# Performance work log

Hardware: AMD Instinct MI355X
Metric: run time of the kernel (lower is better)

Reference implementation:

```python
import jax, jax.numpy as jnp
import numpy as np

BN_EPS = 1e-5


def _conv_bn_elu(x, w, b, bn_scale, bn_bias, bn_mean, bn_var):
    # 1x1 conv == channel-mixing matmul: x [B,C,H,W], w [O,C]
    y = jnp.einsum('bchw,oc->bohw', x, w) + b[None, :, None, None]
    inv = bn_scale * jax.lax.rsqrt(bn_var + BN_EPS)
    y = y * inv[None, :, None, None] + (bn_bias - bn_mean * inv)[None, :, None, None]
    return jax.nn.elu(y)


def setup_inputs() -> dict:
    key = jax.random.key(0)
    ks = jax.random.split(key, 24)
    B, C, H, W = 4, 128, 64, 64
    d = {}
    d['x_q'] = jax.random.normal(ks[0], (B, C, H, W), jnp.float32)
    d['x_k'] = jax.random.normal(ks[1], (B, C, H, W), jnp.float32)
    d['x_v'] = jax.random.normal(ks[2], (B, C, H, W), jnp.float32)
    scale = 1.0 / np.sqrt(C)
    i = 3
    for p in ('q', 'k', 'v'):
        d[f'{p}_w'] = jax.random.normal(ks[i], (C, C), jnp.float32) * scale; i += 1
        d[f'{p}_b'] = jax.random.normal(ks[i], (C,), jnp.float32) * 0.01; i += 1
        d[f'{p}_bn_scale'] = jnp.ones((C,), jnp.float32) + 0.1 * jax.random.normal(ks[i], (C,), jnp.float32); i += 1
        d[f'{p}_bn_bias'] = 0.1 * jax.random.normal(ks[i], (C,), jnp.float32); i += 1
        d[f'{p}_bn_mean'] = 0.1 * jax.random.normal(ks[i], (C,), jnp.float32); i += 1
        d[f'{p}_bn_var'] = jax.random.uniform(ks[i], (C,), jnp.float32, 0.5, 1.5); i += 1
    # torch inits gamma/beta to zero; use small nonzero values so output is informative
    d['gamma'] = jnp.array([0.5], jnp.float32)
    d['beta'] = jnp.array([0.5], jnp.float32)
    return d


def reference(x_q, x_k, x_v,
              q_w, q_b, q_bn_scale, q_bn_bias, q_bn_mean, q_bn_var,
              k_w, k_b, k_bn_scale, k_bn_bias, k_bn_mean, k_bn_var,
              v_w, v_b, v_bn_scale, v_bn_bias, v_bn_mean, v_bn_var,
              gamma, beta):
    B, C, Hv, Wv = x_v.shape
    q = _conv_bn_elu(x_q, q_w, q_b, q_bn_scale, q_bn_bias, q_bn_mean, q_bn_var).reshape(B, C, -1)  # [B,C,HWq]
    k = _conv_bn_elu(x_k, k_w, k_b, k_bn_scale, k_bn_bias, k_bn_mean, k_bn_var).reshape(B, C, -1)  # [B,C,HWk]
    v = _conv_bn_elu(x_v, v_w, v_b, v_bn_scale, v_bn_bias, v_bn_mean, v_bn_var).reshape(B, C, -1)  # [B,C,HWv]
    energy = jnp.einsum('bcq,bck->bqk', q, k)                 # [B,HWq,HWk] (no scaling, as in source)
    attention = jax.nn.softmax(energy, axis=-1)
    out = jnp.einsum('bck,bqk->bcq', v, attention)            # [B,C,HWq]
    out = out.reshape(B, C, Hv, Wv)
    return gamma * out + beta * x_v
```

## Files before the change

### kernel.cpp

```cpp
#include <hip/hip_runtime.h>

#define CC 128
#define SS 4096
#define L2E 1.44269504f

typedef _Float16 f16;
typedef f16 f16x8 __attribute__((ext_vector_type(8)));
typedef float f32x4 __attribute__((ext_vector_type(4)));

struct PArg { const float *x, *w, *b, *sc, *bb, *bm, *bv; f16* out; };

__global__ __launch_bounds__(256) void projk(PArg A0, PArg A1, PArg A2) {
    const int p = blockIdx.y;
    PArg A = (p == 0) ? A0 : ((p == 1) ? A1 : A2);
    const int bx = blockIdx.x;
    const int b  = bx >> 6;
    const int s0 = (bx & 63) * 64;
    const int tid = threadIdx.x;
    const int w = tid >> 6, lane = tid & 63;
    const int n = lane & 15, g = lane >> 4;

    __shared__ f16 Xl[64][136];
    __shared__ f16 Wl[128][136];
    __shared__ float invA[128], ebA[128];
    f16* Yl = &Wl[0][0];

    if (tid < 128) {
        float iv = A.sc[tid] * rsqrtf(A.bv[tid] + 1e-5f);
        invA[tid] = iv;
        ebA[tid] = (A.b[tid] - A.bm[tid]) * iv + A.bb[tid];
    }
#pragma unroll
    for (int i = 0; i < 8; ++i) {
        int vi = tid + i * 256;
        int c = vi >> 4, sq = (vi & 15) * 4;
        float4 v = *(const float4*)(A.x + ((size_t)b * CC + c) * SS + s0 + sq);
        Xl[sq + 0][c] = (f16)v.x; Xl[sq + 1][c] = (f16)v.y;
        Xl[sq + 2][c] = (f16)v.z; Xl[sq + 3][c] = (f16)v.w;
    }
    __syncthreads();
#pragma unroll
    for (int i = 0; i < 8; ++i) {
        int vi = tid + i * 256;
        int o = vi >> 4, cq = (vi & 15) * 8;
        const float* wp = A.w + o * CC + cq;
        float4 a = *(const float4*)wp;
        float4 b4 = *(const float4*)(wp + 4);
        float iv = invA[o];
        union { f16 h[8]; uint4 u; } pk;
        pk.h[0] = (f16)(a.x * iv);  pk.h[1] = (f16)(a.y * iv);
        pk.h[2] = (f16)(a.z * iv);  pk.h[3] = (f16)(a.w * iv);
        pk.h[4] = (f16)(b4.x * iv); pk.h[5] = (f16)(b4.y * iv);
        pk.h[6] = (f16)(b4.z * iv); pk.h[7] = (f16)(b4.w * iv);
        *(uint4*)&Wl[o][cq] = pk.u;
    }
    __syncthreads();

    if (p < 2) {
        f32x4 acc[2][4];
#pragma unroll
        for (int mt = 0; mt < 2; ++mt)
#pragma unroll
            for (int nt = 0; nt < 4; ++nt) acc[mt][nt] = (f32x4){0.f, 0.f, 0.f, 0.f};
#pragma unroll
        for (int ks = 0; ks < 4; ++ks) {
            f16x8 af[2], bf[4];
#pragma unroll
            for (int mt = 0; mt < 2; ++mt) af[mt] = *(const f16x8*)&Wl[w * 32 + mt * 16 + n][ks * 32 + g * 8];
#pragma unroll
            for (int nt = 0; nt < 4; ++nt) bf[nt] = *(const f16x8*)&Xl[nt * 16 + n][ks * 32 + g * 8];
#pragma unroll
            for (int mt = 0; mt < 2; ++mt)
#pragma unroll
                for (int nt = 0; nt < 4; ++nt)
                    acc[mt][nt] = __builtin_amdgcn_mfma_f32_16x16x32_f16(af[mt], bf[nt], acc[mt][nt], 0, 0, 0);
        }
        __syncthreads();
#pragma unroll
        for (int mt = 0; mt < 2; ++mt) {
            float ebr[4];
#pragma unroll
            for (int r = 0; r < 4; ++r) ebr[r] = ebA[w * 32 + mt * 16 + g * 4 + r];
#pragma unroll
            for (int nt = 0; nt < 4; ++nt) {
                union { f16 h[4]; uint2 u; } pk;
#pragma unroll
                for (int r = 0; r < 4; ++r) {
                    float y = acc[mt][nt][r] + ebr[r];
                    y = (y > 0.f) ? y : (expf(y) - 1.f);
                    pk.h[r] = (f16)y;
                }
                *(uint2*)&Yl[(nt * 16 + n) * 136 + w * 32 + mt * 16 + g * 4] = pk.u;
            }
        }
        __syncthreads();
#pragma unroll
        for (int i = 0; i < 4; ++i) {
            int vi = tid + i * 256;
            int s = vi >> 4, cl = (vi & 15) * 8;
            *(uint4*)&A.out[((size_t)b * SS + s0 + s) * CC + cl] = *(const uint4*)&Yl[s * 136 + cl];
        }
    } else {
        f32x4 acc[8];
#pragma unroll
        for (int nt = 0; nt < 8; ++nt) acc[nt] = (f32x4){0.f, 0.f, 0.f, 0.f};
#pragma unroll
        for (int ks = 0; ks < 4; ++ks) {
            f16x8 af = *(const f16x8*)&Xl[w * 16 + n][ks * 32 + g * 8];
#pragma unroll
            for (int nt = 0; nt < 8; ++nt) {
                f16x8 bf = *(const f16x8*)&Wl[nt * 16 + n][ks * 32 + g * 8];
                acc[nt] = __builtin_amdgcn_mfma_f32_16x16x32_f16(af, bf, acc[nt], 0, 0, 0);
            }
        }
        __syncthreads();
#pragma unroll
        for (int nt = 0; nt < 8; ++nt) {
            float ebc = ebA[nt * 16 + n];
            union { f16 h[4]; uint2 u; } pk;
#pragma unroll
            for (int r = 0; r < 4; ++r) {
                float y = acc[nt][r] + ebc;
                y = (y > 0.f) ? y : (expf(y) - 1.f);
                pk.h[r] = (f16)y;
            }
            *(uint2*)&Yl[(nt * 16 + n) * 136 + w * 16 + g * 4] = pk.u;
        }
        __syncthreads();
#pragma unroll
        for (int i = 0; i < 4; ++i) {
            int vi = tid + i * 256;
            int o = vi >> 3, sl = (vi & 7) * 8;
            *(uint4*)&A.out[((size_t)b * CC + o) * SS + s0 + sl] = *(const uint4*)&Yl[o * 136 + sl];
        }
    }
}

__global__ __launch_bounds__(256, 3) void attnk(
    const f16* __restrict__ Qt, const f16* __restrict__ Kt, const f16* __restrict__ Vt,
    f16* __restrict__ Op, float* __restrict__ Ml)
{
    const int tid = threadIdx.x;
    const int bx = blockIdx.x;
    const int qt = bx & 31;
    const int kh = (bx >> 5) & 7;
    const int b  = bx >> 8;
    const int q0 = qt * 128;
    const int kbeg = kh * 512;

    __shared__ __align__(16) char arena[54272];
    f16 (*Kl)[136] = (f16(*)[136])arena;
    f16 (*Vl)[72]  = (f16(*)[72])(arena + 17408);

    const int w = tid >> 6, lane = tid & 63;
    const int n = lane & 15, g = lane >> 4;
    f16 (*Pw)[72] = (f16(*)[72])(arena + 35840 + w * 4608);

    f16x8 qf[2][4];
    {
        const f16* Qb = Qt + ((size_t)b * SS + q0 + w * 32) * CC;
#pragma unroll
        for (int qt2 = 0; qt2 < 2; ++qt2)
#pragma unroll
            for (int ks = 0; ks < 4; ++ks)
                qf[qt2][ks] = *(const f16x8*)&Qb[(qt2 * 16 + n) * CC + ks * 32 + g * 8];
    }

    f32x4 oacc[8][2];
#pragma unroll
    for (int mtc = 0; mtc < 8; ++mtc)
#pragma unroll
        for (int qt2 = 0; qt2 < 2; ++qt2) oacc[mtc][qt2] = (f32x4){0.f, 0.f, 0.f, 0.f};
    float mreg[2] = {-1e30f, -1e30f}, lsum[2] = {0.f, 0.f};

    for (int kt = 0; kt < 8; ++kt) {
        const int k0 = kbeg + kt * 64;
        __syncthreads();
#pragma unroll
        for (int i = 0; i < 4; ++i) {
            int vi = tid + i * 256;
            int rk = vi >> 4, ck = (vi & 15) * 8;
            *(uint4*)&Kl[rk][ck] = *(const uint4*)&Kt[((size_t)b * SS + k0 + rk) * CC + ck];
            int rv = vi >> 3, cv = (vi & 7) * 8;
            *(uint4*)&Vl[rv][cv] = *(const uint4*)&Vt[((size_t)b * CC + rv) * SS + k0 + cv];
        }
        __syncthreads();

        f32x4 sacc[4][2];
#pragma unroll
        for (int kt2 = 0; kt2 < 4; ++kt2)
#pragma unroll
            for (int qt2 = 0; qt2 < 2; ++qt2) sacc[kt2][qt2] = (f32x4){0.f, 0.f, 0.f, 0.f};
#pragma unroll
        for (int ks = 0; ks < 4; ++ks) {
            f16x8 kf[4];
#pragma unroll
            for (int kt2 = 0; kt2 < 4; ++kt2) kf[kt2] = *(const f16x8*)&Kl[kt2 * 16 + n][ks * 32 + g * 8];
#pragma unroll
            for (int kt2 = 0; kt2 < 4; ++kt2)
#pragma unroll
                for (int qt2 = 0; qt2 < 2; ++qt2)
                    sacc[kt2][qt2] = __builtin_amdgcn_mfma_f32_16x16x32_f16(kf[kt2], qf[qt2][ks], sacc[kt2][qt2], 0, 0, 0);
        }

        float al[2];
#pragma unroll
        for (int qt2 = 0; qt2 < 2; ++qt2) {
            float v = sacc[0][qt2][0];
#pragma unroll
            for (int kt2 = 0; kt2 < 4; ++kt2)
#pragma unroll
                for (int r = 0; r < 4; ++r) v = fmaxf(v, sacc[kt2][qt2][r]);
            v = fmaxf(v, __shfl_xor(v, 16));
            v = fmaxf(v, __shfl_xor(v, 32));
            float mn = fmaxf(mreg[qt2], v);
            al[qt2] = exp2f((mreg[qt2] - mn) * L2E);
            mreg[qt2] = mn;
            float rs = 0.f;
#pragma unroll
            for (int kt2 = 0; kt2 < 4; ++kt2) {
                union { f16 h[4]; uint2 u; } pk;
#pragma unroll
                for (int r = 0; r < 4; ++r) {
                    float p = exp2f((sacc[kt2][qt2][r] - mn) * L2E);
                    rs += p;
                    pk.h[r] = (f16)p;
                }
                *(uint2*)&Pw[qt2 * 16 + n][kt2 * 16 + g * 4] = pk.u;
            }
            lsum[qt2] = lsum[qt2] * al[qt2] + rs;
        }
#pragma unroll
        for (int mtc = 0; mtc < 8; ++mtc)
#pragma unroll
            for (int qt2 = 0; qt2 < 2; ++qt2)
#pragma unroll
                for (int r = 0; r < 4; ++r) oacc[mtc][qt2][r] *= al[qt2];

#pragma unroll
        for (int ks = 0; ks < 2; ++ks) {
            f16x8 vf[8], pf[2];
#pragma unroll
            for (int mtc = 0; mtc < 8; ++mtc) vf[mtc] = *(const f16x8*)&Vl[mtc * 16 + n][ks * 32 + g * 8];
#pragma unroll
            for (int qt2 = 0; qt2 < 2; ++qt2) pf[qt2] = *(const f16x8*)&Pw[qt2 * 16 + n][ks * 32 + g * 8];
#pragma unroll
            for (int mtc = 0; mtc < 8; ++mtc)
#pragma unroll
                for (int qt2 = 0; qt2 < 2; ++qt2)
                    oacc[mtc][qt2] = __builtin_amdgcn_mfma_f32_16x16x32_f16(vf[mtc], pf[qt2], oacc[mtc][qt2], 0, 0, 0);
        }
    }

    float lreg[2];
#pragma unroll
    for (int qt2 = 0; qt2 < 2; ++qt2) {
        float s = lsum[qt2];
        s += __shfl_xor(s, 16);
        s += __shfl_xor(s, 32);
        lreg[qt2] = s;
    }

    const int pidx = (b * 32 + qt) * 8 + kh;
    if (g == 0) {
        float* MlW = Ml + (size_t)pidx * 256;
#pragma unroll
        for (int qt2 = 0; qt2 < 2; ++qt2) {
            int q = w * 32 + qt2 * 16 + n;
            MlW[q]       = mreg[qt2];
            MlW[128 + q] = lreg[qt2];
        }
    }

    __syncthreads();
    f16 (*S2)[136] = (f16(*)[136])arena;
#pragma unroll
    for (int mtc = 0; mtc < 8; ++mtc)
#pragma unroll
        for (int qt2 = 0; qt2 < 2; ++qt2)
#pragma unroll
            for (int r = 0; r < 4; ++r)
                S2[mtc * 16 + g * 4 + r][w * 32 + qt2 * 16 + n] = (f16)oacc[mtc][qt2][r];
    __syncthreads();
    f16* OpW = Op + (size_t)pidx * 16384;
#pragma unroll
    for (int i = 0; i < 8; ++i) {
        int vi = tid + i * 256;
        int c = vi >> 4, qq = (vi & 15) * 8;
        *(uint4*)&OpW[c * 128 + qq] = *(const uint4*)&S2[c][qq];
    }
}

__global__ __launch_bounds__(256) void mrgk(
    const f16* __restrict__ Op, const float* __restrict__ Ml,
    const float* __restrict__ xv, const float* __restrict__ gp, const float* __restrict__ bp,
    float* __restrict__ out)
{
    const int bx = blockIdx.x;
    const int cg = bx & 3, bqt = bx >> 2;
    const int b = bqt >> 5, qt = bqt & 31;
    const int tid = threadIdx.x;
    const int q = tid & 127, hf = tid >> 7;

    const float* ml = Ml + (size_t)bqt * 8 * 256;
    float m = -1e30f;
#pragma unroll
    for (int k2 = 0; k2 < 8; ++k2) m = fmaxf(m, ml[k2 * 256 + q]);
    float wt[8], tot = 0.f;
#pragma unroll
    for (int k2 = 0; k2 < 8; ++k2) {
        wt[k2] = exp2f((ml[k2 * 256 + q] - m) * L2E);
        tot += wt[k2] * ml[k2 * 256 + 128 + q];
    }
    float inv = 1.f / tot;
    float gm = gp[0], bb = bp[0];

    const f16* O = Op + (size_t)bqt * 8 * 16384;
#pragma unroll 2
    for (int i = 0; i < 16; ++i) {
        int c = cg * 32 + hf * 16 + i;
        float o = 0.f;
#pragma unroll
        for (int k2 = 0; k2 < 8; ++k2) o += wt[k2] * (float)O[k2 * 16384 + c * 128 + q];
        o *= inv;
        size_t idx = ((size_t)(b * CC + c)) * SS + qt * 128 + q;
        out[idx] = gm * o + bb * xv[idx];
    }
}

extern "C" void kernel_launch(void* const* d_in, const int* in_sizes, int n_in,
                              void* d_out, int out_size, void* d_ws, size_t ws_size,
                              hipStream_t stream) {
    (void)in_sizes; (void)n_in; (void)out_size; (void)ws_size;

    const size_t TEN = (size_t)4 * SS * CC;
    f16* Qt = (f16*)d_ws;
    f16* Kt = Qt + TEN;
    f16* Vt = Kt + TEN;
    f16* Op = Vt + TEN;
    float* Ml = (float*)(Op + (size_t)1024 * 16384);

    PArg aq = { (const float*)d_in[0], (const float*)d_in[3],  (const float*)d_in[4],
                (const float*)d_in[5], (const float*)d_in[6],  (const float*)d_in[7],
                (const float*)d_in[8],  Qt };
    PArg ak = { (const float*)d_in[1], (const float*)d_in[9],  (const float*)d_in[10],
                (const float*)d_in[11], (const float*)d_in[12], (const float*)d_in[13],
                (const float*)d_in[14], Kt };
    PArg av = { (const float*)d_in[2], (const float*)d_in[15], (const float*)d_in[16],
                (const float*)d_in[17], (const float*)d_in[18], (const float*)d_in[19],
                (const float*)d_in[20], Vt };

    hipLaunchKernelGGL(projk, dim3(256, 3), dim3(256), 0, stream, aq, ak, av);
    hipLaunchKernelGGL(attnk, dim3(1024), dim3(256), 0, stream, Qt, Kt, Vt, Op, Ml);
    hipLaunchKernelGGL(mrgk, dim3(512), dim3(256), 0, stream,
                       Op, Ml, (const float*)d_in[2], (const float*)d_in[21],
                       (const float*)d_in[22], (float*)d_out);
}
```

Measured before the change: 215.9 us.

## Drop split-K attention and merge kernel; fuse epilogue and prefetch K/V tiles

Replaces the split-key flash attention (8 key partitions per query tile plus a separate merge kernel) with one block per 64-query tile that walks all 4096 keys. The gamma/beta epilogue is fused into the attention kernel, so the f16 partial-output workspace and the merge launch go away. K/V tiles for the next step are now prefetched into registers. In exchange the grid shrinks from 1024 to 256 blocks, each wave handles only 16 queries, and per-block serial work is longer, so the GPU may be underoccupied and each K/V tile feeds fewer MFMAs.

```diff
diff --git a/kernel.cpp b/kernel.cpp
--- a/kernel.cpp
+++ b/kernel.cpp
@@ -136,61 +136,74 @@
     }
 }
 
-__global__ __launch_bounds__(256, 3) void attnk(
+__global__ __launch_bounds__(256) void attnk(
     const f16* __restrict__ Qt, const f16* __restrict__ Kt, const f16* __restrict__ Vt,
-    f16* __restrict__ Op, float* __restrict__ Ml)
+    const float* __restrict__ xv, const float* __restrict__ gp, const float* __restrict__ bp,
+    float* __restrict__ out)
 {
     const int tid = threadIdx.x;
     const int bx = blockIdx.x;
-    const int qt = bx & 31;
-    const int kh = (bx >> 5) & 7;
-    const int b  = bx >> 8;
-    const int q0 = qt * 128;
-    const int kbeg = kh * 512;
-
-    __shared__ __align__(16) char arena[54272];
+    const int b  = bx >> 6;
+    const int qt = bx & 63;
+    const int q0 = qt * 64;
+
+    __shared__ __align__(16) char arena[45056];
     f16 (*Kl)[136] = (f16(*)[136])arena;
     f16 (*Vl)[72]  = (f16(*)[72])(arena + 17408);
 
     const int w = tid >> 6, lane = tid & 63;
     const int n = lane & 15, g = lane >> 4;
-    f16 (*Pw)[72] = (f16(*)[72])(arena + 35840 + w * 4608);
-
-    f16x8 qf[2][4];
+    f16 (*Pw)[72] = (f16(*)[72])(arena + 35840 + w * 2304);
+
+    f16x8 qf[4];
     {
-        const f16* Qb = Qt + ((size_t)b * SS + q0 + w * 32) * CC;
-#pragma unroll
-        for (int qt2 = 0; qt2 < 2; ++qt2)
-#pragma unroll
-            for (int ks = 0; ks < 4; ++ks)
-                qf[qt2][ks] = *(const f16x8*)&Qb[(qt2 * 16 + n) * CC + ks * 32 + g * 8];
-    }
-
-    f32x4 oacc[8][2];
-#pragma unroll
-    for (int mtc = 0; mtc < 8; ++mtc)
-#pragma unroll
-        for (int qt2 = 0; qt2 < 2; ++qt2) oacc[mtc][qt2] = (f32x4){0.f, 0.f, 0.f, 0.f};
-    float mreg[2] = {-1e30f, -1e30f}, lsum[2] = {0.f, 0.f};
-
-    for (int kt = 0; kt < 8; ++kt) {
-        const int k0 = kbeg + kt * 64;
+        const f16* Qb = Qt + ((size_t)b * SS + q0 + w * 16 + n) * CC;
+#pragma unroll
+        for (int ks = 0; ks < 4; ++ks)
+            qf[ks] = *(const f16x8*)&Qb[ks * 32 + g * 8];
+    }
+
+    f32x4 oacc[8];
+#pragma unroll
+    for (int mtc = 0; mtc < 8; ++mtc) oacc[mtc] = (f32x4){0.f, 0.f, 0.f, 0.f};
+    float mreg = -1e30f, lsum = 0.f;
+
+    uint4 pk4[4], pv4[4];
+#pragma unroll
+    for (int i = 0; i < 4; ++i) {
+        int vi = tid + i * 256;
+        int rk = vi >> 4, ck = (vi & 15) * 8;
+        pk4[i] = *(const uint4*)&Kt[((size_t)b * SS + rk) * CC + ck];
+        int rv = vi >> 3, cv = (vi & 7) * 8;
+        pv4[i] = *(const uint4*)&Vt[((size_t)b * CC + rv) * SS + cv];
+    }
+
+    for (int kt = 0; kt < 64; ++kt) {
         __syncthreads();
 #pragma unroll
         for (int i = 0; i < 4; ++i) {
             int vi = tid + i * 256;
             int rk = vi >> 4, ck = (vi & 15) * 8;
-            *(uint4*)&Kl[rk][ck] = *(const uint4*)&Kt[((size_t)b * SS + k0 + rk) * CC + ck];
+            *(uint4*)&Kl[rk][ck] = pk4[i];
             int rv = vi >> 3, cv = (vi & 7) * 8;
-            *(uint4*)&Vl[rv][cv] = *(const uint4*)&Vt[((size_t)b * CC + rv) * SS + k0 + cv];
-        }
-        __syncthreads();
-
-        f32x4 sacc[4][2];
-#pragma unroll
-        for (int kt2 = 0; kt2 < 4; ++kt2)
-#pragma unroll
-            for (int qt2 = 0; qt2 < 2; ++qt2) sacc[kt2][qt2] = (f32x4){0.f, 0.f, 0.f, 0.f};
+            *(uint4*)&Vl[rv][cv] = pv4[i];
+        }
+        if (kt < 63) {
+            const int k1 = (kt + 1) * 64;
+#pragma unroll
+            for (int i = 0; i < 4; ++i) {
+                int vi = tid + i * 256;
+                int rk = vi >> 4, ck = (vi & 15) * 8;
+                pk4[i] = *(const uint4*)&Kt[((size_t)b * SS + k1 + rk) * CC + ck];
+                int rv = vi >> 3, cv = (vi & 7) * 8;
+                pv4[i] = *(const uint4*)&Vt[((size_t)b * CC + rv) * SS + k1 + cv];
+            }
+        }
+        __syncthreads();
+
+        f32x4 sacc[4];
+#pragma unroll
+        for (int kt2 = 0; kt2 < 4; ++kt2) sacc[kt2] = (f32x4){0.f, 0.f, 0.f, 0.f};
 #pragma unroll
         for (int ks = 0; ks < 4; ++ks) {
             f16x8 kf[4];
@@ -198,133 +211,72 @@
             for (int kt2 = 0; kt2 < 4; ++kt2) kf[kt2] = *(const f16x8*)&Kl[kt2 * 16 + n][ks * 32 + g * 8];
 #pragma unroll
             for (int kt2 = 0; kt2 < 4; ++kt2)
-#pragma unroll
-                for (int qt2 = 0; qt2 < 2; ++qt2)
-                    sacc[kt2][qt2] = __builtin_amdgcn_mfma_f32_16x16x32_f16(kf[kt2], qf[qt2][ks], sacc[kt2][qt2], 0, 0, 0);
-        }
-
-        float al[2];
-#pragma unroll
-        for (int qt2 = 0; qt2 < 2; ++qt2) {
-            float v = sacc[0][qt2][0];
-#pragma unroll
-            for (int kt2 = 0; kt2 < 4; ++kt2)
-#pragma unroll
-                for (int r = 0; r < 4; ++r) v = fmaxf(v, sacc[kt2][qt2][r]);
-            v = fmaxf(v, __shfl_xor(v, 16));
-            v = fmaxf(v, __shfl_xor(v, 32));
-            float mn = fmaxf(mreg[qt2], v);
-            al[qt2] = exp2f((mreg[qt2] - mn) * L2E);
-            mreg[qt2] = mn;
-            float rs = 0.f;
-#pragma unroll
-            for (int kt2 = 0; kt2 < 4; ++kt2) {
-                union { f16 h[4]; uint2 u; } pk;
-#pragma unroll
-                for (int r = 0; r < 4; ++r) {
-                    float p = exp2f((sacc[kt2][qt2][r] - mn) * L2E);
-                    rs += p;
-                    pk.h[r] = (f16)p;
-                }
-                *(uint2*)&Pw[qt2 * 16 + n][kt2 * 16 + g * 4] = pk.u;
-            }
-            lsum[qt2] = lsum[qt2] * al[qt2] + rs;
-        }
+                sacc[kt2] = __builtin_amdgcn_mfma_f32_16x16x32_f16(kf[kt2], qf[ks], sacc[kt2], 0, 0, 0);
+        }
+
+        float v = sacc[0][0];
+#pragma unroll
+        for (int kt2 = 0; kt2 < 4; ++kt2)
+#pragma unroll
+            for (int r = 0; r < 4; ++r) v = fmaxf(v, sacc[kt2][r]);
+        v = fmaxf(v, __shfl_xor(v, 16));
+        v = fmaxf(v, __shfl_xor(v, 32));
+        float mn = fmaxf(mreg, v);
+        float al = exp2f((mreg - mn) * L2E);
+        mreg = mn;
+        float rs = 0.f;
+#pragma unroll
+        for (int kt2 = 0; kt2 < 4; ++kt2) {
+            union { f16 h[4]; uint2 u; } pk;
+#pragma unroll
+            for (int r = 0; r < 4; ++r) {
+                float p = exp2f((sacc[kt2][r] - mn) * L2E);
+                rs += p;
+                pk.h[r] = (f16)p;
+            }
+            *(uint2*)&Pw[n][kt2 * 16 + g * 4] = pk.u;
+        }
+        lsum = lsum * al + rs;
 #pragma unroll
         for (int mtc = 0; mtc < 8; ++mtc)
 #pragma unroll
-            for (int qt2 = 0; qt2 < 2; ++qt2)
-#pragma unroll
-                for (int r = 0; r < 4; ++r) oacc[mtc][qt2][r] *= al[qt2];
+            for (int r = 0; r < 4; ++r) oacc[mtc][r] *= al;
 
 #pragma unroll
         for (int ks = 0; ks < 2; ++ks) {
-            f16x8 vf[8], pf[2];
-#pragma unroll
-            for (int mtc = 0; mtc < 8; ++mtc) vf[mtc] = *(const f16x8*)&Vl[mtc * 16 + n][ks * 32 + g * 8];
-#pragma unroll
-            for (int qt2 = 0; qt2 < 2; ++qt2) pf[qt2] = *(const f16x8*)&Pw[qt2 * 16 + n][ks * 32 + g * 8];
-#pragma unroll
-            for (int mtc = 0; mtc < 8; ++mtc)
-#pragma unroll
-                for (int qt2 = 0; qt2 < 2; ++qt2)
-                    oacc[mtc][qt2] = __builtin_amdgcn_mfma_f32_16x16x32_f16(vf[mtc], pf[qt2], oacc[mtc][qt2], 0, 0, 0);
-        }
-    }
-
-    float lreg[2];
-#pragma unroll
-    for (int qt2 = 0; qt2 < 2; ++qt2) {
-        float s = lsum[qt2];
-        s += __shfl_xor(s, 16);
-        s += __shfl_xor(s, 32);
-        lreg[qt2] = s;
-    }
-
-    const int pidx = (b * 32 + qt) * 8 + kh;
-    if (g == 0) {
-        float* MlW = Ml + (size_t)pidx * 256;
-#pragma unroll
-        for (int qt2 = 0; qt2 < 2; ++qt2) {
-            int q = w * 32 + qt2 * 16 + n;
-            MlW[q]       = mreg[qt2];
-            MlW[128 + q] = lreg[qt2];
-        }
-    }
+            f16x8 pf = *(const f16x8*)&Pw[n][ks * 32 + g * 8];
+#pragma unroll
+            for (int mtc = 0; mtc < 8; ++mtc) {
+                f16x8 vf = *(const f16x8*)&Vl[mtc * 16 + n][ks * 32 + g * 8];
+                oacc[mtc] = __builtin_amdgcn_mfma_f32_16x16x32_f16(vf, pf, oacc[mtc], 0, 0, 0);
+            }
+        }
+    }
+
+    float s = lsum;
+    s += __shfl_xor(s, 16);
+    s += __shfl_xor(s, 32);
+    float linv = 1.f / s;
+    float gm = gp[0], bb = bp[0];
 
     __syncthreads();
-    f16 (*S2)[136] = (f16(*)[136])arena;
+    float (*S2f)[68] = (float(*)[68])arena;
 #pragma unroll
     for (int mtc = 0; mtc < 8; ++mtc)
 #pragma unroll
-        for (int qt2 = 0; qt2 < 2; ++qt2)
-#pragma unroll
-            for (int r = 0; r < 4; ++r)
-                S2[mtc * 16 + g * 4 + r][w * 32 + qt2 * 16 + n] = (f16)oacc[mtc][qt2][r];
+        for (int r = 0; r < 4; ++r)
+            S2f[mtc * 16 + g * 4 + r][w * 16 + n] = gm * oacc[mtc][r] * linv;
     __syncthreads();
-    f16* OpW = Op + (size_t)pidx * 16384;
 #pragma unroll
     for (int i = 0; i < 8; ++i) {
         int vi = tid + i * 256;
-        int c = vi >> 4, qq = (vi & 15) * 8;
-        *(uint4*)&OpW[c * 128 + qq] = *(const uint4*)&S2[c][qq];
-    }
-}
-
-__global__ __launch_bounds__(256) void mrgk(
-    const f16* __restrict__ Op, const float* __restrict__ Ml,
-    const float* __restrict__ xv, const float* __restrict__ gp, const float* __restrict__ bp,
-    float* __restrict__ out)
-{
-    const int bx = blockIdx.x;
-    const int cg = bx & 3, bqt = bx >> 2;
-    const int b = bqt >> 5, qt = bqt & 31;
-    const int tid = threadIdx.x;
-    const int q = tid & 127, hf = tid >> 7;
-
-    const float* ml = Ml + (size_t)bqt * 8 * 256;
-    float m = -1e30f;
-#pragma unroll
-    for (int k2 = 0; k2 < 8; ++k2) m = fmaxf(m, ml[k2 * 256 + q]);
-    float wt[8], tot = 0.f;
-#pragma unroll
-    for (int k2 = 0; k2 < 8; ++k2) {
-        wt[k2] = exp2f((ml[k2 * 256 + q] - m) * L2E);
-        tot += wt[k2] * ml[k2 * 256 + 128 + q];
-    }
-    float inv = 1.f / tot;
-    float gm = gp[0], bb = bp[0];
-
-    const f16* O = Op + (size_t)bqt * 8 * 16384;
-#pragma unroll 2
-    for (int i = 0; i < 16; ++i) {
-        int c = cg * 32 + hf * 16 + i;
-        float o = 0.f;
-#pragma unroll
-        for (int k2 = 0; k2 < 8; ++k2) o += wt[k2] * (float)O[k2 * 16384 + c * 128 + q];
-        o *= inv;
-        size_t idx = ((size_t)(b * CC + c)) * SS + qt * 128 + q;
-        out[idx] = gm * o + bb * xv[idx];
+        int c = vi >> 4, qq = (vi & 15) * 4;
+        size_t idx = ((size_t)(b * CC + c)) * SS + q0 + qq;
+        float4 xvv = *(const float4*)&xv[idx];
+        float4 ov = *(const float4*)&S2f[c][qq];
+        ov.x += bb * xvv.x; ov.y += bb * xvv.y;
+        ov.z += bb * xvv.z; ov.w += bb * xvv.w;
+        *(float4*)&out[idx] = ov;
     }
 }
 
@@ -337,8 +289,6 @@
     f16* Qt = (f16*)d_ws;
     f16* Kt = Qt + TEN;
     f16* Vt = Kt + TEN;
-    f16* Op = Vt + TEN;
-    float* Ml = (float*)(Op + (size_t)1024 * 16384);
 
     PArg aq = { (const float*)d_in[0], (const float*)d_in[3],  (const float*)d_in[4],
                 (const float*)d_in[5], (const float*)d_in[6],  (const float*)d_in[7],
@@ -351,8 +301,7 @@
                 (const float*)d_in[20], Vt };
 
     hipLaunchKernelGGL(projk, dim3(256, 3), dim3(256), 0, stream, aq, ak, av);
-    hipLaunchKernelGGL(attnk, dim3(1024), dim3(256), 0, stream, Qt, Kt, Vt, Op, Ml);
-    hipLaunchKernelGGL(mrgk, dim3(512), dim3(256), 0, stream,
-                       Op, Ml, (const float*)d_in[2], (const float*)d_in[21],
-                       (const float*)d_in[22], (float*)d_out);
+    hipLaunchKernelGGL(attnk, dim3(256), dim3(256), 0, stream, Qt, Kt, Vt,
+                       (const float*)d_in[2], (const float*)d_in[21], (const float*)d_in[22],
+                       (float*)d_out);
 }
```

New measurement: 413.0 us. +91.2%, slower.
